# Kernel optimization log

Hardware: AMD Instinct MI355X
Metric: run time of the kernel (lower is better)

The kernel has to match this reference:

```python
import jax, jax.numpy as jnp
import numpy as np

H = 16        # num_heads
K = 128       # head_k_dim
V = 128       # head_v_dim (expand_v = 1.0)
BT = 64       # chunk_size
BASE_LR = 0.1
EPS = 1e-05


def setup_inputs() -> dict:
    key = jax.random.key(0)
    ks = jax.random.split(key, 9)
    B, T, D = 2, 4096, 2048
    s = 0.02
    inputs = jax.random.normal(ks[0], (B, T, D), jnp.float32)
    Wq = jax.random.normal(ks[1], (H * K, D), jnp.float32) * s
    Wk = jax.random.normal(ks[2], (H * K, D), jnp.float32) * s
    Wv = jax.random.normal(ks[3], (H * V, D), jnp.float32) * s
    Weta = jax.random.normal(ks[4], (H, D), jnp.float32) * s
    Wtheta = jax.random.normal(ks[5], (H, D), jnp.float32) * s
    Wg = jax.random.normal(ks[6], (H * V, D), jnp.float32) * s
    norm_w = jnp.ones((V,), jnp.float32)
    Wo = jax.random.normal(ks[7], (D, H * V), jnp.float32) * s
    return {"inputs": inputs, "Wq": Wq, "Wk": Wk, "Wv": Wv, "Weta": Weta,
            "Wtheta": Wtheta, "Wg": Wg, "norm_w": norm_w, "Wo": Wo}


def _forward(inputs, Wq, Wk, Wv, Weta, Wtheta, Wg, norm_w, Wo):
    B, T, D = inputs.shape

    def proj_heads(W, d):
        # (B,T,D) @ (D,H*d) -> (B,H,T,d)
        return (inputs @ W.T).reshape(B, T, H, d).transpose(0, 2, 1, 3)

    q = proj_heads(Wq, K) * (K ** -0.5)
    k = proj_heads(Wk, K)
    v = proj_heads(Wv, V)

    eta = jax.nn.sigmoid(inputs @ Weta.T).transpose(0, 2, 1)          # (B,H,T)
    theta = BASE_LR * jax.nn.sigmoid(inputs @ Wtheta.T).transpose(0, 2, 1)

    NT = T // BT

    def chunkify(x, d):
        return x.reshape(B, H, NT, BT, d).transpose(2, 0, 1, 3, 4)    # (NT,B,H,BT,d)

    qs, kc_all, vs = chunkify(q, K), chunkify(k, K), chunkify(v, V)
    es = eta.reshape(B, H, NT, BT).transpose(2, 0, 1, 3)              # (NT,B,H,BT)
    ts = theta.reshape(B, H, NT, BT).transpose(2, 0, 1, 3)

    tril = jnp.tril(jnp.ones((BT, BT), bool))

    def step(W, xs):
        # W: (B,H,V,K) matrix-valued fast-weight state
        qc, kc, vc, ec, tc = xs
        e = jnp.einsum('bhtk,bhvk->bhtv', kc, W) - vc                  # prediction error
        lec = jnp.cumsum(jnp.log(jnp.clip(ec, 1e-8, None)), axis=-1)   # (B,H,BT) cum log-decay
        beta = jnp.where(tril,
                         jnp.exp(jnp.minimum(lec[..., :, None] - lec[..., None, :], 0.0)),
                         0.0)                                          # (B,H,BT,BT)
        qk = jnp.einsum('bhik,bhjk->bhij', qc, kc)
        theta_e = tc[..., None] * e                                    # (B,H,BT,V)
        z = (jnp.einsum('bhtk,bhvk->bhtv', qc * jnp.exp(lec)[..., None], W)
             - jnp.einsum('bhij,bhjv->bhiv', qk * beta, theta_e))
        e_decay = beta[:, :, -1, :, None] * theta_e                    # decay-to-chunk-end
        dw = jnp.einsum('bhtv,bhtk->bhvk', e_decay, kc)
        Wn = W * jnp.exp(lec[..., -1])[..., None, None] - dw
        return Wn, z

    W0 = jnp.zeros((B, H, V, K), inputs.dtype)
    W_fin, outs = jax.lax.scan(step, W0, (qs, kc_all, vs, es, ts))     # outs: (NT,B,H,BT,V)
    outs = outs.transpose(1, 2, 0, 3, 4).reshape(B, H, T, V).transpose(0, 2, 1, 3)  # (B,T,H,V)

    # gated RMS norm: rmsnorm(x) * weight * silu(g)
    g = (inputs @ Wg.T).reshape(B, T, H, V)
    rms = outs * jax.lax.rsqrt(jnp.mean(outs * outs, axis=-1, keepdims=True) + EPS)
    o = rms * norm_w * jax.nn.silu(g)
    return o.reshape(B, T, H * V) @ Wo.T                               # (B,T,D)


def reference(inputs, Wq, Wk, Wv, Weta, Wtheta, Wg, norm_w, Wo):
    return _forward(inputs, Wq, Wk, Wv, Weta, Wtheta, Wg, norm_w, Wo)
```

## Files before the change

kernel.cpp:

```cpp
#include <hip/hip_runtime.h>
#include <cstdint>
#include <cstddef>


typedef unsigned short u16b;
typedef uint32_t u32;
typedef __attribute__((ext_vector_type(8))) __bf16 bf16x8;
typedef __attribute__((ext_vector_type(4))) float  f32x4;

__device__ __forceinline__ float bf2f(u16b v){
  union { float f; uint32_t u; } x; x.u = ((uint32_t)v) << 16; return x.f;
}
__device__ __forceinline__ void split2(float f, u16b& h, u16b& l){
  uint32_t u = __float_as_uint(f);
  float hf = __uint_as_float(u & 0xFFFF0000u);
  h = (u16b)(u >> 16);
  l = (u16b)(__float_as_uint(f - hf) >> 16);
}
__device__ __forceinline__ f32x4 mfma16(bf16x8 a, bf16x8 b, f32x4 c){
  return __builtin_amdgcn_mfma_f32_16x16x32_bf16(a, b, c, 0, 0, 0);
}
__device__ __forceinline__ void gl16(const void* g, void* l){
  __builtin_amdgcn_global_load_lds(
      (const __attribute__((address_space(1))) u32*)g,
      (__attribute__((address_space(3))) u32*)l, 16, 0, 0);
}
__device__ __forceinline__ int ksw(int r, int c){
  return r*128 + (c ^ ((r & 7) << 3));
}

__global__ __launch_bounds__(256) void split_kernel(
    const float* __restrict__ src, u16b* __restrict__ dh, u16b* __restrict__ dl,
    int n8)
{
  int i = blockIdx.x*256 + threadIdx.x;
  if (i >= n8) return;
  const float4* s4 = (const float4*)src;
  float4 a = s4[2*(size_t)i], b = s4[2*(size_t)i + 1];
  float f[8] = {a.x,a.y,a.z,a.w,b.x,b.y,b.z,b.w};
  u16b h[8], l[8];
#pragma unroll
  for (int j = 0; j < 8; j++) split2(f[j], h[j], l[j]);
  *(uint4*)(dh + (size_t)i*8) = *(const uint4*)h;
  *(uint4*)(dl + (size_t)i*8) = *(const uint4*)l;
}

template<int BMODE, int OUTMODE>
__global__ __launch_bounds__(256) void gemm3v(
    const u16b* __restrict__ Ah, const u16b* __restrict__ Al,
    const u16b* __restrict__ Bh, const u16b* __restrict__ Bl,
    const float* __restrict__ Bf,
    u16b* __restrict__ Ch, u16b* __restrict__ Cl, float* __restrict__ Cf,
    int M, int N, int Kd, float alpha)
{
  (void)M;
  __shared__ __align__(16) u16b smem[16384];
  u16b* Ahs = smem;
  u16b* Als = smem + 4096;
  u16b* Bhs = smem + 8192;
  u16b* Bls = smem + 12288;

  const int cpx = gridDim.x >> 3;
  const int flat = blockIdx.x;
  const int swz = (flat & 7) * cpx + (flat >> 3);
  const int nb = N >> 7;
  const int m0 = (swz / nb) * 128;
  const int n0 = (swz % nb) * 128;

  const int tid  = threadIdx.x;
  const int wid  = tid >> 6;
  const int lane = tid & 63;
  const int wm = (wid & 1) * 64;
  const int wn = (wid >> 1) * 64;
  const int rw = lane & 15;
  const int kq = (lane >> 4) * 8;
  const int sx = ((rw >> 1) & 3) << 3;

  const int srow = tid >> 2;
  const int scol = ((tid & 3) * 8) ^ (((tid >> 3) & 3) << 3);
  const u16b* gA0 = Ah + (size_t)(m0 + srow)*Kd + scol;
  const u16b* gA1 = gA0 + (size_t)64*Kd;
  const u16b* gAl0 = Al + (size_t)(m0 + srow)*Kd + scol;
  const u16b* gAl1 = gAl0 + (size_t)64*Kd;
  const u16b* gB0 = nullptr; const u16b* gB1 = nullptr;
  const u16b* gBl0 = nullptr; const u16b* gBl1 = nullptr;
  if constexpr (BMODE == 1){
    gB0  = Bh + (size_t)(n0 + srow)*Kd + scol;
    gB1  = gB0 + (size_t)64*Kd;
    gBl0 = Bl + (size_t)(n0 + srow)*Kd + scol;
    gBl1 = gBl0 + (size_t)64*Kd;
  }

  f32x4 acc[4][4] = {};

  for (int k0 = 0; k0 < Kd; k0 += 32){
    float4 fb[4];
    if constexpr (BMODE == 0){
#pragma unroll
      for (int it = 0; it < 4; it++){
        int idx = it*256 + tid;
        int rr = idx >> 3, c4 = (idx & 7) * 4;
        fb[it] = *(const float4*)(Bf + (size_t)(n0 + rr) * Kd + k0 + c4);
      }
    }
    __syncthreads();
    gl16(gA0  + k0, Ahs + tid*8);
    gl16(gA1  + k0, Ahs + 2048 + tid*8);
    gl16(gAl0 + k0, Als + tid*8);
    gl16(gAl1 + k0, Als + 2048 + tid*8);
    if constexpr (BMODE == 1){
      gl16(gB0  + k0, Bhs + tid*8);
      gl16(gB1  + k0, Bhs + 2048 + tid*8);
      gl16(gBl0 + k0, Bls + tid*8);
      gl16(gBl1 + k0, Bls + 2048 + tid*8);
    } else {
#pragma unroll
      for (int it = 0; it < 4; it++){
        int idx = it*256 + tid;
        int rr = idx >> 3, c4 = (idx & 7) * 4;
        int cs = c4 ^ (((rr >> 1) & 3) << 3);
        float f[4] = {fb[it].x, fb[it].y, fb[it].z, fb[it].w};
        u16b h[4], l[4];
#pragma unroll
        for (int j = 0; j < 4; j++) split2(f[j], h[j], l[j]);
        *(uint2*)&Bhs[rr*32 + cs] = *(const uint2*)h;
        *(uint2*)&Bls[rr*32 + cs] = *(const uint2*)l;
      }
    }
    __syncthreads();

    bf16x8 afh[4], afl[4], bfh[4], bfl[4];
#pragma unroll
    for (int i = 0; i < 4; i++){
      afh[i] = *(const bf16x8*)&Ahs[(wm + i*16 + rw)*32 + (kq ^ sx)];
      afl[i] = *(const bf16x8*)&Als[(wm + i*16 + rw)*32 + (kq ^ sx)];
    }
#pragma unroll
    for (int j = 0; j < 4; j++){
      bfh[j] = *(const bf16x8*)&Bhs[(wn + j*16 + rw)*32 + (kq ^ sx)];
      bfl[j] = *(const bf16x8*)&Bls[(wn + j*16 + rw)*32 + (kq ^ sx)];
    }
#pragma unroll
    for (int i = 0; i < 4; i++)
#pragma unroll
      for (int j = 0; j < 4; j++){
        f32x4 t = mfma16(afl[i], bfh[j], acc[i][j]);
        t = mfma16(afh[i], bfl[j], t);
        acc[i][j] = mfma16(afh[i], bfh[j], t);
      }
  }

  float* Bnc = (float*)smem;
  const int ccol  = lane & 15;
  const int cquad = lane >> 4;
  const int brb = ((wid & 1) << 4) + cquad*4;
  const int br2 = tid >> 3, c0 = (tid & 7) * 16;
#pragma unroll
  for (int i = 0; i < 4; i++){
    __syncthreads();
#pragma unroll
    for (int j = 0; j < 4; j++)
#pragma unroll
      for (int r = 0; r < 4; r++)
        Bnc[(brb + r)*132 + wn + j*16 + ccol] = acc[i][j][r];
    __syncthreads();
    const int rowg = m0 + ((br2 >> 4) << 6) + i*16 + (br2 & 15);
    float4 x0 = *(const float4*)&Bnc[br2*132 + c0];
    float4 x1 = *(const float4*)&Bnc[br2*132 + c0 + 4];
    float4 x2 = *(const float4*)&Bnc[br2*132 + c0 + 8];
    float4 x3 = *(const float4*)&Bnc[br2*132 + c0 + 12];
    float v[16] = {x0.x,x0.y,x0.z,x0.w, x1.x,x1.y,x1.z,x1.w,
                   x2.x,x2.y,x2.z,x2.w, x3.x,x3.y,x3.z,x3.w};
#pragma unroll
    for (int e = 0; e < 16; e++) v[e] *= alpha;
    if constexpr (OUTMODE == 0){
      u16b h[16], l[16];
#pragma unroll
      for (int e = 0; e < 16; e++) split2(v[e], h[e], l[e]);
      size_t off = (size_t)rowg * N + n0 + c0;
      *(uint4*)(Ch + off)     = *(const uint4*)&h[0];
      *(uint4*)(Ch + off + 8) = *(const uint4*)&h[8];
      *(uint4*)(Cl + off)     = *(const uint4*)&l[0];
      *(uint4*)(Cl + off + 8) = *(const uint4*)&l[8];
    } else {
      size_t off = (size_t)rowg * N + n0 + c0;
      *(float4*)(Cf + off)      = *(const float4*)&v[0];
      *(float4*)(Cf + off + 4)  = *(const float4*)&v[4];
      *(float4*)(Cf + off + 8)  = *(const float4*)&v[8];
      *(float4*)(Cf + off + 12) = *(const float4*)&v[12];
    }
  }
}

__global__ __launch_bounds__(256) void etatheta_kernel(
    const float* __restrict__ x, const float* __restrict__ Weta,
    const float* __restrict__ Wtheta, float* __restrict__ eta, float* __restrict__ theta)
{
  __shared__ float xr[2048];
  const int bt = blockIdx.x;
  const int b = bt >> 12, t = bt & 4095;
  const float* xp = x + (size_t)bt * 2048;
  for (int i = threadIdx.x; i < 2048; i += 256) xr[i] = xp[i];
  __syncthreads();
  const int wid = threadIdx.x >> 6, lane = threadIdx.x & 63;
  for (int oi = 0; oi < 8; oi++){
    int og = wid*8 + oi;
    const float* wrow = (og < 16) ? (Weta + (size_t)og*2048)
                                  : (Wtheta + (size_t)(og-16)*2048);
    float acc = 0.f;
    for (int d = lane; d < 2048; d += 64) acc += xr[d] * wrow[d];
#pragma unroll
    for (int off = 32; off; off >>= 1) acc += __shfl_down(acc, off);
    if (lane == 0){
      float s = 1.f / (1.f + expf(-acc));
      if (og < 16) eta  [((size_t)(b*16 + og     ))*4096 + t] = s;
      else         theta[((size_t)(b*16 + og - 16))*4096 + t] = 0.1f * s;
    }
  }
}

__global__ __launch_bounds__(64) void decay_kernel(
    const float* __restrict__ eta, const float* __restrict__ th,
    float* __restrict__ lecb, float* __restrict__ eltb, float* __restrict__ wtb)
{
  const int bh = blockIdx.x, n = blockIdx.y, lane = threadIdx.x;
  size_t idx = (size_t)bh*4096 + n*64 + lane;
  float cum = logf(fmaxf(eta[idx], 1e-8f));
#pragma unroll
  for (int off = 1; off < 64; off <<= 1){
    float o = __shfl_up(cum, off);
    if (lane >= off) cum += o;
  }
  float lec63 = __shfl(cum, 63);
  lecb[idx] = cum;
  eltb[idx] = expf(cum);
  wtb[idx]  = expf(lec63 - cum) * th[idx];
}

#define WSTR 136
__global__ __launch_bounds__(512) void scan_kernel(
    const u16b* __restrict__ qh, const u16b* __restrict__ ql,
    const u16b* __restrict__ kh, const u16b* __restrict__ kl,
    const float* __restrict__ lecb, const float* __restrict__ eltb,
    const float* __restrict__ wtb,  const float* __restrict__ thb,
    float* vo)
{
  __shared__ u16b kh_s[64*128], kl_s[64*128];
  __shared__ u16b kTh_s[128*72], kTl_s[128*72];
  __shared__ u16b Wh[32*WSTR], Wl[32*WSTR];
  __shared__ u16b eh_s [32*72], el_s [32*72];
  __shared__ u16b ewh_s[32*72], ewl_s[32*72];
  __shared__ u16b Sh_s [64*72], Sl_s [64*72];
  __shared__ float v_s[64*36];
  __shared__ float dec_s[4*64];

  const int bh = blockIdx.x;
  const int b = bh >> 4, h = bh & 15;
  const int v0 = blockIdx.y * 32;
  const int tid  = threadIdx.x;
  const int wid  = tid >> 6;
  const int tw   = wid & 3;
  const int jh   = wid >> 2;
  const int lane = tid & 63;
  const int rw = lane & 15;
  const int kq = (lane >> 4) * 8;
  const int ccol  = lane & 15;
  const int cquad = lane >> 4;

  for (int i = tid; i < 32*WSTR; i += 512){ Wh[i] = 0; Wl[i] = 0; }

  const size_t rowbase = (size_t)b * 4096;
  const size_t decbase = (size_t)bh * 4096;
  const int sr0 = tid >> 4;
  const int sc8 = (tid & 15) * 8;
  const int rot = ((tid & 15) + ((lane >> 4) << 1)) & 7;

  for (int n = 0; n < 64; n++){
    const int tbase = n * 64;
    __syncthreads();

#pragma unroll
    for (int it = 0; it < 2; it++){
      int r = it*32 + sr0;
      size_t g = (rowbase + tbase + r) * 2048 + (size_t)h*128 + sc8;
      uint4 uh = *(const uint4*)&kh[g];
      uint4 ul = *(const uint4*)&kl[g];
      *(uint4*)&kh_s[ksw(r, sc8)] = uh;
      *(uint4*)&kl_s[ksw(r, sc8)] = ul;
      const u16b* ph = (const u16b*)&uh;
      const u16b* pl = (const u16b*)&ul;
#pragma unroll
      for (int s = 0; s < 8; s++){
        int i = (s + rot) & 7;
        kTh_s[(sc8 + i)*72 + r] = ph[i];
        kTl_s[(sc8 + i)*72 + r] = pl[i];
      }
    }
    {
      int r = tid >> 3, c4 = (tid & 7) * 4;
      size_t g = (rowbase + tbase + r) * 2048 + (size_t)h*128 + v0 + c4;
      *(float4*)&v_s[r*36 + c4] = *(const float4*)&vo[g];
    }
    if (tid < 256){
      const float* srcs[4] = {lecb, eltb, wtb, thb};
      dec_s[tid] = srcs[tid >> 6][decbase + tbase + (tid & 63)];
    }
    const size_t qg = (rowbase + tbase + tw*16 + rw) * 2048 + (size_t)h*128;
    bf16x8 qah[4], qal[4];
#pragma unroll
    for (int ks = 0; ks < 4; ks++){
      qah[ks] = *(const bf16x8*)(qh + qg + ks*32 + kq);
      qal[ks] = *(const bf16x8*)(ql + qg + ks*32 + kq);
    }
    __syncthreads();

    f32x4 eacc = {};
#pragma unroll
    for (int ks = 0; ks < 4; ks++){
      bf16x8 ah  = *(const bf16x8*)&kh_s[ksw(tw*16 + rw, ks*32 + kq)];
      bf16x8 al  = *(const bf16x8*)&kl_s[ksw(tw*16 + rw, ks*32 + kq)];
      bf16x8 bh_ = *(const bf16x8*)&Wh[(jh*16 + rw)*WSTR + ks*32 + kq];
      bf16x8 bl_ = *(const bf16x8*)&Wl[(jh*16 + rw)*WSTR + ks*32 + kq];
      f32x4 t = mfma16(al, bh_, eacc);
      t = mfma16(ah, bl_, t);
      eacc = mfma16(ah, bh_, t);
    }
    f32x4 qkacc[2] = {};
    f32x4 zqacc = {};
#pragma unroll
    for (int ks = 0; ks < 4; ks++){
#pragma unroll
      for (int j2 = 0; j2 < 2; j2++){
        int j4 = jh*2 + j2;
        bf16x8 bh_ = *(const bf16x8*)&kh_s[ksw(j4*16 + rw, ks*32 + kq)];
        bf16x8 bl_ = *(const bf16x8*)&kl_s[ksw(j4*16 + rw, ks*32 + kq)];
        f32x4 t = mfma16(qal[ks], bh_, qkacc[j2]);
        t = mfma16(qah[ks], bl_, t);
        qkacc[j2] = mfma16(qah[ks], bh_, t);
      }
      bf16x8 wh_ = *(const bf16x8*)&Wh[(jh*16 + rw)*WSTR + ks*32 + kq];
      bf16x8 wl_ = *(const bf16x8*)&Wl[(jh*16 + rw)*WSTR + ks*32 + kq];
      f32x4 t = mfma16(qal[ks], wh_, zqacc);
      t = mfma16(qah[ks], wl_, t);
      zqacc = mfma16(qah[ks], wh_, t);
    }
#pragma unroll
    for (int r = 0; r < 4; r++){
      int t  = tw*16 + cquad*4 + r;
      int vv = jh*16 + ccol;
      float e = eacc[r] - v_s[t*36 + vv];
      u16b h1, l1; split2(e, h1, l1);
      eh_s[vv*72 + t] = h1;  el_s[vv*72 + t] = l1;
      float ew = e * dec_s[128 + t];
      u16b h2, l2; split2(ew, h2, l2);
      ewh_s[vv*72 + t] = h2; ewl_s[vv*72 + t] = l2;
    }
#pragma unroll
    for (int j2 = 0; j2 < 2; j2++)
#pragma unroll
      for (int r = 0; r < 4; r++){
        int t  = tw*16 + cquad*4 + r;
        int jj = (jh*2 + j2)*16 + ccol;
        float s = 0.f;
        if (jj <= t)
          s = qkacc[j2][r] * __expf(fminf(dec_s[t] - dec_s[jj], 0.f)) * dec_s[192 + jj];
        u16b h1, l1; split2(s, h1, l1);
        Sh_s[t*72 + jj] = h1;  Sl_s[t*72 + jj] = l1;
      }
    __syncthreads();

    f32x4 seacc = {};
#pragma unroll
    for (int ks2 = 0; ks2 < 2; ks2++){
      bf16x8 ah  = *(const bf16x8*)&Sh_s[(tw*16 + rw)*72 + ks2*32 + kq];
      bf16x8 al  = *(const bf16x8*)&Sl_s[(tw*16 + rw)*72 + ks2*32 + kq];
      bf16x8 bh_ = *(const bf16x8*)&eh_s[(jh*16 + rw)*72 + ks2*32 + kq];
      bf16x8 bl_ = *(const bf16x8*)&el_s[(jh*16 + rw)*72 + ks2*32 + kq];
      f32x4 t = mfma16(al, bh_, seacc);
      t = mfma16(ah, bl_, t);
      seacc = mfma16(ah, bh_, t);
    }
#pragma unroll
    for (int r = 0; r < 4; r++){
      int t  = tw*16 + cquad*4 + r;
      int vv = jh*16 + ccol;
      float z = dec_s[64 + t]*zqacc[r] - seacc[r];
      vo[((rowbase + tbase + t)*16 + h)*128 + v0 + vv] = z;
    }
    f32x4 dwacc[2] = {};
    const int kcol = wid*16 + rw;
#pragma unroll
    for (int ks2 = 0; ks2 < 2; ks2++){
      bf16x8 bh_ = *(const bf16x8*)&kTh_s[kcol*72 + ks2*32 + kq];
      bf16x8 bl_ = *(const bf16x8*)&kTl_s[kcol*72 + ks2*32 + kq];
#pragma unroll
      for (int mi = 0; mi < 2; mi++){
        bf16x8 amh = *(const bf16x8*)&ewh_s[(mi*16 + rw)*72 + ks2*32 + kq];
        bf16x8 aml = *(const bf16x8*)&ewl_s[(mi*16 + rw)*72 + ks2*32 + kq];
        f32x4 t = mfma16(aml, bh_, dwacc[mi]);
        t = mfma16(amh, bl_, t);
        dwacc[mi] = mfma16(amh, bh_, t);
      }
    }
    float dfac = dec_s[64 + 63];
#pragma unroll
    for (int mi = 0; mi < 2; mi++)
#pragma unroll
      for (int r = 0; r < 4; r++){
        int vv = mi*16 + cquad*4 + r;
        int kk = wid*16 + ccol;
        int idx = vv*WSTR + kk;
        float w = bf2f(Wh[idx]) + bf2f(Wl[idx]);
        w = w*dfac - dwacc[mi][r];
        u16b h1, l1; split2(w, h1, l1);
        Wh[idx] = h1; Wl[idx] = l1;
      }
  }
}
#undef WSTR

__global__ __launch_bounds__(256) void norm_kernel(
    const float* __restrict__ outs, const float* __restrict__ g,
    const float* __restrict__ nw, u16b* __restrict__ ogh, u16b* __restrict__ ogl)
{
  const int bt = blockIdx.x;
  const int tid = threadIdx.x;
  size_t base = (size_t)bt*2048 + (size_t)tid*8;
  float4 x0 = *(const float4*)(outs + base);
  float4 x1 = *(const float4*)(outs + base + 4);
  float x[8] = {x0.x,x0.y,x0.z,x0.w,x1.x,x1.y,x1.z,x1.w};
  float ss = 0.f;
#pragma unroll
  for (int i = 0; i < 8; i++) ss += x[i]*x[i];
#pragma unroll
  for (int off = 1; off < 16; off <<= 1) ss += __shfl_xor(ss, off);
  float rs = rsqrtf(ss*(1.f/128.f) + 1e-5f);
  float4 g0 = *(const float4*)(g + base);
  float4 g1 = *(const float4*)(g + base + 4);
  float gg[8] = {g0.x,g0.y,g0.z,g0.w,g1.x,g1.y,g1.z,g1.w};
  int nwb = (tid & 15)*8;
  u16b oh[8], ol[8];
#pragma unroll
  for (int i = 0; i < 8; i++){
    float sig = 1.f / (1.f + __expf(-gg[i]));
    float v = x[i]*rs*nw[nwb+i]*gg[i]*sig;
    split2(v, oh[i], ol[i]);
  }
  *(uint4*)(ogh + base) = *(const uint4*)oh;
  *(uint4*)(ogl + base) = *(const uint4*)ol;
}

extern "C" void kernel_launch(void* const* d_in, const int* in_sizes, int n_in,
                              void* d_out, int out_size, void* d_ws, size_t ws_size,
                              hipStream_t stream)
{
  (void)in_sizes; (void)n_in; (void)out_size; (void)ws_size;
  const float* x    = (const float*)d_in[0];
  const float* Wq   = (const float*)d_in[1];
  const float* Wk   = (const float*)d_in[2];
  const float* Wv   = (const float*)d_in[3];
  const float* Weta = (const float*)d_in[4];
  const float* Wth  = (const float*)d_in[5];
  const float* Wg   = (const float*)d_in[6];
  const float* nw   = (const float*)d_in[7];
  const float* Wo   = (const float*)d_in[8];
  float* out = (float*)d_out;

  const size_t SZ = (size_t)8192*2048;
  const size_t WZ = (size_t)2048*2048;
  const size_t DS = (size_t)2*16*4096;
  u16b* ws = (u16b*)d_ws;
  u16b* qhb = ws;            u16b* qlb = qhb + SZ;
  u16b* khb = qlb + SZ;      u16b* klb = khb + SZ;
  float* vob  = (float*)(klb + SZ);
  float* etab = vob + SZ;
  float* thb  = etab + DS;
  float* lecb = thb  + DS;
  float* eltb = lecb + DS;
  float* wtb  = eltb + DS;
  float* gfb  = (float*)khb;
  u16b* ogh = qhb; u16b* ogl = qlb;

  u16b* xh = (u16b*)d_out;   u16b* xl = xh + SZ;
  u16b* wsQh = khb;        u16b* wsQl = khb + WZ;
  u16b* wsKh = (u16b*)vob; u16b* wsKl = wsKh + WZ;
  u16b* wsGh = qhb;        u16b* wsGl = qhb + WZ;
  u16b* wsOh = khb;        u16b* wsOl = khb + WZ;

  dim3 gg(1024);
  split_kernel<<<8192, 256, 0, stream>>>(x, xh, xl, (int)(SZ/8));
  etatheta_kernel<<<8192, 256, 0, stream>>>(x, Weta, Wth, etab, thb);
  decay_kernel<<<dim3(32,64), 64, 0, stream>>>(etab, thb, lecb, eltb, wtb);

  split_kernel<<<2048, 256, 0, stream>>>(Wq, wsQh, wsQl, (int)(WZ/8));
  gemm3v<1,0><<<gg, 256, 0, stream>>>(xh, xl, wsQh, wsQl, nullptr,
                                      qhb, qlb, nullptr,
                                      8192, 2048, 2048, 0.08838834764831843f);
  split_kernel<<<2048, 256, 0, stream>>>(Wk, wsKh, wsKl, (int)(WZ/8));
  gemm3v<1,0><<<gg, 256, 0, stream>>>(xh, xl, wsKh, wsKl, nullptr,
                                      khb, klb, nullptr,
                                      8192, 2048, 2048, 1.f);
  gemm3v<0,1><<<gg, 256, 0, stream>>>(xh, xl, nullptr, nullptr, Wv,
                                      nullptr, nullptr, vob,
                                      8192, 2048, 2048, 1.f);
  scan_kernel<<<dim3(32,4), 512, 0, stream>>>(qhb, qlb, khb, klb,
                                              lecb, eltb, wtb, thb, vob);
  split_kernel<<<2048, 256, 0, stream>>>(Wg, wsGh, wsGl, (int)(WZ/8));
  gemm3v<1,1><<<gg, 256, 0, stream>>>(xh, xl, wsGh, wsGl, nullptr,
                                      nullptr, nullptr, gfb,
                                      8192, 2048, 2048, 1.f);
  norm_kernel<<<8192, 256, 0, stream>>>(vob, gfb, nw, ogh, ogl);
  split_kernel<<<2048, 256, 0, stream>>>(Wo, wsOh, wsOl, (int)(WZ/8));
  gemm3v<1,1><<<gg, 256, 0, stream>>>(ogh, ogl, wsOh, wsOl, nullptr,
                                      nullptr, nullptr, out,
                                      8192, 2048, 2048, 1.f);
}
```

Baseline: 1.842 ms.

## Prefetch next chunk into registers and pack hi/lo bf16 pairs in LDS

Global loads of k, v, decay values and q for the next chunk are now issued into registers during the current chunk's compute, so load latency can hide behind the MFMA work of the scan. The transposed k, e and e-weighted buffers are stored as packed 32-bit hi/lo pairs with XOR swizzles and unpacked with byte-perm instructions. The S buffer also gets a swizzle. Together these aim to cut LDS bank conflicts and the many scalar 16-bit stores, in exchange for higher register pressure and extra perm ALU work.

```diff
diff --git a/kernel.cpp b/kernel.cpp
--- a/kernel.cpp
+++ b/kernel.cpp
@@ -27,6 +27,20 @@
 }
 __device__ __forceinline__ int ksw(int r, int c){
   return r*128 + (c ^ ((r & 7) << 3));
+}
+__device__ __forceinline__ void unpack8(const u32* p, bf16x8& hv, bf16x8& lv){
+  uint4 P0 = *(const uint4*)p;
+  uint4 P1 = *(const uint4*)(p + 4);
+  union { u32 w[4]; bf16x8 v; } H, L;
+  H.w[0] = __builtin_amdgcn_perm(P0.y, P0.x, 0x07060302u);
+  H.w[1] = __builtin_amdgcn_perm(P0.w, P0.z, 0x07060302u);
+  H.w[2] = __builtin_amdgcn_perm(P1.y, P1.x, 0x07060302u);
+  H.w[3] = __builtin_amdgcn_perm(P1.w, P1.z, 0x07060302u);
+  L.w[0] = __builtin_amdgcn_perm(P0.y, P0.x, 0x05040100u);
+  L.w[1] = __builtin_amdgcn_perm(P0.w, P0.z, 0x05040100u);
+  L.w[2] = __builtin_amdgcn_perm(P1.y, P1.x, 0x05040100u);
+  L.w[3] = __builtin_amdgcn_perm(P1.w, P1.z, 0x05040100u);
+  hv = H.v; lv = L.v;
 }
 
 __global__ __launch_bounds__(256) void split_kernel(
@@ -246,11 +260,11 @@
     float* vo)
 {
   __shared__ u16b kh_s[64*128], kl_s[64*128];
-  __shared__ u16b kTh_s[128*72], kTl_s[128*72];
+  __shared__ u32  kTp[128*68];
   __shared__ u16b Wh[32*WSTR], Wl[32*WSTR];
-  __shared__ u16b eh_s [32*72], el_s [32*72];
-  __shared__ u16b ewh_s[32*72], ewl_s[32*72];
-  __shared__ u16b Sh_s [64*72], Sl_s [64*72];
+  __shared__ u32  epk [32*68];
+  __shared__ u32  ewpk[32*68];
+  __shared__ u16b Sh_s[64*72], Sl_s[64*72];
   __shared__ float v_s[64*36];
   __shared__ float dec_s[4*64];
 
@@ -273,7 +287,35 @@
   const size_t decbase = (size_t)bh * 4096;
   const int sr0 = tid >> 4;
   const int sc8 = (tid & 15) * 8;
-  const int rot = ((tid & 15) + ((lane >> 4) << 1)) & 7;
+  const int vr  = tid >> 3;
+  const int vc4 = (tid & 7) * 4;
+  const float* dsrc = (tid < 64) ? lecb : (tid < 128) ? eltb
+                     : (tid < 192) ? wtb : thb;
+  const size_t doff = decbase + (tid & 63);
+
+  uint4 kuh[2], kul[2];
+  float4 vreg;
+  float dreg = 0.f;
+  bf16x8 qch[4], qcl[4];
+
+  {
+#pragma unroll
+    for (int it = 0; it < 2; it++){
+      int r = it*32 + sr0;
+      size_t g = (rowbase + r) * 2048 + (size_t)h*128 + sc8;
+      kuh[it] = *(const uint4*)&kh[g];
+      kul[it] = *(const uint4*)&kl[g];
+    }
+    { size_t g = (rowbase + vr) * 2048 + (size_t)h*128 + v0 + vc4;
+      vreg = *(const float4*)&vo[g]; }
+    dreg = dsrc[doff];
+    const size_t qg0 = (rowbase + tw*16 + rw) * 2048 + (size_t)h*128;
+#pragma unroll
+    for (int ks = 0; ks < 4; ks++){
+      qch[ks] = *(const bf16x8*)(qh + qg0 + ks*32 + kq);
+      qcl[ks] = *(const bf16x8*)(ql + qg0 + ks*32 + kq);
+    }
+  }
 
   for (int n = 0; n < 64; n++){
     const int tbase = n * 64;
@@ -282,37 +324,37 @@
 #pragma unroll
     for (int it = 0; it < 2; it++){
       int r = it*32 + sr0;
-      size_t g = (rowbase + tbase + r) * 2048 + (size_t)h*128 + sc8;
-      uint4 uh = *(const uint4*)&kh[g];
-      uint4 ul = *(const uint4*)&kl[g];
-      *(uint4*)&kh_s[ksw(r, sc8)] = uh;
-      *(uint4*)&kl_s[ksw(r, sc8)] = ul;
-      const u16b* ph = (const u16b*)&uh;
-      const u16b* pl = (const u16b*)&ul;
-#pragma unroll
-      for (int s = 0; s < 8; s++){
-        int i = (s + rot) & 7;
-        kTh_s[(sc8 + i)*72 + r] = ph[i];
-        kTl_s[(sc8 + i)*72 + r] = pl[i];
-      }
-    }
-    {
-      int r = tid >> 3, c4 = (tid & 7) * 4;
-      size_t g = (rowbase + tbase + r) * 2048 + (size_t)h*128 + v0 + c4;
-      *(float4*)&v_s[r*36 + c4] = *(const float4*)&vo[g];
-    }
-    if (tid < 256){
-      const float* srcs[4] = {lecb, eltb, wtb, thb};
-      dec_s[tid] = srcs[tid >> 6][decbase + tbase + (tid & 63)];
-    }
-    const size_t qg = (rowbase + tbase + tw*16 + rw) * 2048 + (size_t)h*128;
-    bf16x8 qah[4], qal[4];
-#pragma unroll
-    for (int ks = 0; ks < 4; ks++){
-      qah[ks] = *(const bf16x8*)(qh + qg + ks*32 + kq);
-      qal[ks] = *(const bf16x8*)(ql + qg + ks*32 + kq);
-    }
-    __syncthreads();
+      *(uint4*)&kh_s[ksw(r, sc8)] = kuh[it];
+      *(uint4*)&kl_s[ksw(r, sc8)] = kul[it];
+      const u32* hw = (const u32*)&kuh[it];
+      const u32* lw = (const u32*)&kul[it];
+      const int kx = ((sc8 >> 3) & 3) << 3;
+#pragma unroll
+      for (int w = 0; w < 4; w++){
+        u32 pe = __builtin_amdgcn_perm(hw[w], lw[w], 0x05040100u);
+        u32 po = __builtin_amdgcn_perm(hw[w], lw[w], 0x07060302u);
+        int c0 = sc8 + 2*w;
+        kTp[c0*68 + (r ^ kx)]     = pe;
+        kTp[(c0+1)*68 + (r ^ kx)] = po;
+      }
+    }
+    *(float4*)&v_s[vr*36 + vc4] = vreg;
+    if (tid < 256) dec_s[tid] = dreg;
+    __syncthreads();
+
+    if (n < 63){
+      const int tb2 = tbase + 64;
+#pragma unroll
+      for (int it = 0; it < 2; it++){
+        int r = it*32 + sr0;
+        size_t g = (rowbase + tb2 + r) * 2048 + (size_t)h*128 + sc8;
+        kuh[it] = *(const uint4*)&kh[g];
+        kul[it] = *(const uint4*)&kl[g];
+      }
+      { size_t g = (rowbase + tb2 + vr) * 2048 + (size_t)h*128 + v0 + vc4;
+        vreg = *(const float4*)&vo[g]; }
+      dreg = dsrc[doff + tb2];
+    }
 
     f32x4 eacc = {};
 #pragma unroll
@@ -334,26 +376,47 @@
         int j4 = jh*2 + j2;
         bf16x8 bh_ = *(const bf16x8*)&kh_s[ksw(j4*16 + rw, ks*32 + kq)];
         bf16x8 bl_ = *(const bf16x8*)&kl_s[ksw(j4*16 + rw, ks*32 + kq)];
-        f32x4 t = mfma16(qal[ks], bh_, qkacc[j2]);
-        t = mfma16(qah[ks], bl_, t);
-        qkacc[j2] = mfma16(qah[ks], bh_, t);
+        f32x4 t = mfma16(qcl[ks], bh_, qkacc[j2]);
+        t = mfma16(qch[ks], bl_, t);
+        qkacc[j2] = mfma16(qch[ks], bh_, t);
       }
       bf16x8 wh_ = *(const bf16x8*)&Wh[(jh*16 + rw)*WSTR + ks*32 + kq];
       bf16x8 wl_ = *(const bf16x8*)&Wl[(jh*16 + rw)*WSTR + ks*32 + kq];
-      f32x4 t = mfma16(qal[ks], wh_, zqacc);
-      t = mfma16(qah[ks], wl_, t);
-      zqacc = mfma16(qah[ks], wh_, t);
-    }
-#pragma unroll
-    for (int r = 0; r < 4; r++){
-      int t  = tw*16 + cquad*4 + r;
-      int vv = jh*16 + ccol;
-      float e = eacc[r] - v_s[t*36 + vv];
-      u16b h1, l1; split2(e, h1, l1);
-      eh_s[vv*72 + t] = h1;  el_s[vv*72 + t] = l1;
-      float ew = e * dec_s[128 + t];
-      u16b h2, l2; split2(ew, h2, l2);
-      ewh_s[vv*72 + t] = h2; ewl_s[vv*72 + t] = l2;
+      f32x4 t = mfma16(qcl[ks], wh_, zqacc);
+      t = mfma16(qch[ks], wl_, t);
+      zqacc = mfma16(qch[ks], wh_, t);
+    }
+    if (n < 63){
+      const size_t qg2 = (rowbase + tbase + 64 + tw*16 + rw) * 2048 + (size_t)h*128;
+#pragma unroll
+      for (int ks = 0; ks < 4; ks++){
+        qch[ks] = *(const bf16x8*)(qh + qg2 + ks*32 + kq);
+        qcl[ks] = *(const bf16x8*)(ql + qg2 + ks*32 + kq);
+      }
+    }
+    {
+      const int vv = jh*16 + ccol;
+      const int t0 = tw*16 + cquad*4;
+      u32 pe[4], pw[4];
+#pragma unroll
+      for (int r = 0; r < 4; r++){
+        int t = t0 + r;
+        float e = eacc[r] - v_s[t*36 + vv];
+        u16b h1, l1; split2(e, h1, l1);
+        pe[r] = ((u32)h1 << 16) | l1;
+        float ew = e * dec_s[128 + t];
+        u16b h2, l2; split2(ew, h2, l2);
+        pw[r] = ((u32)h2 << 16) | l2;
+      }
+      const int tS = t0 ^ ((vv & 7) << 3);
+      uint2 w0; w0.x = pe[0]; w0.y = pe[1];
+      uint2 w1; w1.x = pe[2]; w1.y = pe[3];
+      *(uint2*)&epk[vv*68 + tS]     = w0;
+      *(uint2*)&epk[vv*68 + tS + 2] = w1;
+      uint2 w2; w2.x = pw[0]; w2.y = pw[1];
+      uint2 w3; w3.x = pw[2]; w3.y = pw[3];
+      *(uint2*)&ewpk[vv*68 + tS]     = w2;
+      *(uint2*)&ewpk[vv*68 + tS + 2] = w3;
     }
 #pragma unroll
     for (int j2 = 0; j2 < 2; j2++)
@@ -365,17 +428,22 @@
         if (jj <= t)
           s = qkacc[j2][r] * __expf(fminf(dec_s[t] - dec_s[jj], 0.f)) * dec_s[192 + jj];
         u16b h1, l1; split2(s, h1, l1);
-        Sh_s[t*72 + jj] = h1;  Sl_s[t*72 + jj] = l1;
+        int jjs = jj ^ (((t >> 2) & 7) << 3);
+        Sh_s[t*72 + jjs] = h1;  Sl_s[t*72 + jjs] = l1;
       }
     __syncthreads();
 
     f32x4 seacc = {};
 #pragma unroll
     for (int ks2 = 0; ks2 < 2; ks2++){
-      bf16x8 ah  = *(const bf16x8*)&Sh_s[(tw*16 + rw)*72 + ks2*32 + kq];
-      bf16x8 al  = *(const bf16x8*)&Sl_s[(tw*16 + rw)*72 + ks2*32 + kq];
-      bf16x8 bh_ = *(const bf16x8*)&eh_s[(jh*16 + rw)*72 + ks2*32 + kq];
-      bf16x8 bl_ = *(const bf16x8*)&el_s[(jh*16 + rw)*72 + ks2*32 + kq];
+      const int srow = tw*16 + rw;
+      const int scol = (ks2*32 + kq) ^ (((srow >> 2) & 7) << 3);
+      bf16x8 ah = *(const bf16x8*)&Sh_s[srow*72 + scol];
+      bf16x8 al = *(const bf16x8*)&Sl_s[srow*72 + scol];
+      const int erow = jh*16 + rw;
+      const int ecol = (ks2*32 + kq) ^ ((erow & 7) << 3);
+      bf16x8 bh_, bl_;
+      unpack8(&epk[erow*68 + ecol], bh_, bl_);
       f32x4 t = mfma16(al, bh_, seacc);
       t = mfma16(ah, bl_, t);
       seacc = mfma16(ah, bh_, t);
@@ -389,14 +457,17 @@
     }
     f32x4 dwacc[2] = {};
     const int kcol = wid*16 + rw;
+    const int kx2  = ((kcol >> 3) & 3) << 3;
 #pragma unroll
     for (int ks2 = 0; ks2 < 2; ks2++){
-      bf16x8 bh_ = *(const bf16x8*)&kTh_s[kcol*72 + ks2*32 + kq];
-      bf16x8 bl_ = *(const bf16x8*)&kTl_s[kcol*72 + ks2*32 + kq];
+      bf16x8 bh_, bl_;
+      unpack8(&kTp[kcol*68 + ((ks2*32 + kq) ^ kx2)], bh_, bl_);
 #pragma unroll
       for (int mi = 0; mi < 2; mi++){
-        bf16x8 amh = *(const bf16x8*)&ewh_s[(mi*16 + rw)*72 + ks2*32 + kq];
-        bf16x8 aml = *(const bf16x8*)&ewl_s[(mi*16 + rw)*72 + ks2*32 + kq];
+        const int arow = mi*16 + rw;
+        const int acol = (ks2*32 + kq) ^ ((arow & 7) << 3);
+        bf16x8 amh, aml;
+        unpack8(&ewpk[arow*68 + acol], amh, aml);
         f32x4 t = mfma16(aml, bh_, dwacc[mi]);
         t = mfma16(amh, bl_, t);
         dwacc[mi] = mfma16(amh, bh_, t);
```

Measured after the change: 1.771 ms. 1.04x faster.
